# Kernel optimization log

Measured on AMD Instinct MI355X. Metric: run time of the kernel, lower is better.

## Reference

```python
import jax, jax.numpy as jnp
import numpy as np

N_BISECT_ITERS = 50  # entmax library default


def entmax_bisect(X, alpha, n_iter=N_BISECT_ITERS):
    """alpha-entmax over last axis via bisection (Peters & Martins 2019).
    Solves for tau s.t. sum(max((alpha-1)X - tau, 0)^(1/(alpha-1))) = 1."""
    am1 = alpha - 1.0
    inv = 1.0 / am1
    Xa = X * am1
    max_val = jnp.max(Xa, axis=-1, keepdims=True)
    d = X.shape[-1]
    tau_lo = max_val - 1.0                                   # _gp(1, alpha) = 1
    tau_hi = max_val - jnp.asarray(1.0 / d, X.dtype) ** am1  # _gp(1/d, alpha)

    def pfun(tau):
        return jnp.maximum(Xa - tau, 0.0) ** inv

    f_lo = jnp.sum(pfun(tau_lo), axis=-1, keepdims=True) - 1.0

    def body(i, carry):
        tau_lo, dm = carry
        dm = dm * 0.5
        tau_m = tau_lo + dm
        f_m = jnp.sum(pfun(tau_m), axis=-1, keepdims=True) - 1.0
        tau_lo = jnp.where(f_m * f_lo >= 0, tau_m, tau_lo)
        return (tau_lo, dm)

    tau_lo, _ = jax.lax.fori_loop(0, n_iter, body, (tau_lo, tau_hi - tau_lo))
    p = pfun(tau_lo)
    return p / jnp.sum(p, axis=-1, keepdims=True)  # ensure_sum_one


def setup_inputs() -> dict:
    master = jax.random.key(0)
    kq, kk, kv = jax.random.split(master, 3)
    B, H, S, D = 4, 16, 2048, 64
    return {
        "query": jax.random.normal(kq, (B, H, S, D), jnp.float32),
        "key": jax.random.normal(kk, (B, H, S, D), jnp.float32),
        "value": jax.random.normal(kv, (B, H, S, D), jnp.float32),
        "alpha": jnp.float32(1.5),  # canonical entmax-1.5
    }


def reference(query, key, value, alpha):
    D = query.shape[-1]
    scale = 1.0 / jnp.sqrt(jnp.asarray(D, query.dtype))
    scores = jnp.einsum('bhqd,bhkd->bhqk', query, key) * scale  # [B,H,S,S]
    p_attn = entmax_bisect(scores, alpha)
    out = jnp.einsum('bhqk,bhkd->bhqd', p_attn, value)
    return (out, p_attn)
```

## Files before the change

kernel.cpp:

```cpp
#include <hip/hip_runtime.h>
#include <math.h>

#define S_LEN 2048
#define HD    64
#define QT    16
#define NT    1024
#define NW    16
#define NTIL  8
#define CAP   512
#define NITER 28
#define NEWT  10

typedef short s8v __attribute__((ext_vector_type(8)));
typedef float f4v __attribute__((ext_vector_type(4)));

template <bool B> struct BoolT { static constexpr bool value = B; };

__device__ __forceinline__ float wave_sum(float v) {
#pragma unroll
    for (int off = 32; off >= 1; off >>= 1)
        v += __shfl_xor(v, off, 64);
    return v;
}

__device__ __forceinline__ float group16_max(float v) {
#pragma unroll
    for (int off = 8; off >= 1; off >>= 1)
        v = fmaxf(v, __shfl_xor(v, off, 64));
    return v;
}

__device__ __forceinline__ unsigned f2bf2(float lo, float hi) {
    unsigned a = __float_as_uint(lo), b = __float_as_uint(hi);
    a += 0x7FFFu + ((a >> 16) & 1u);
    b += 0x7FFFu + ((b >> 16) & 1u);
    return (a >> 16) | (b & 0xFFFF0000u);
}

__device__ __forceinline__ s8v pack_bf8(const float4& x, const float4& y, float sc) {
    union { s8v s; unsigned u[4]; } f;
    f.u[0] = f2bf2(x.x * sc, x.y * sc);
    f.u[1] = f2bf2(x.z * sc, x.w * sc);
    f.u[2] = f2bf2(y.x * sc, y.y * sc);
    f.u[3] = f2bf2(y.z * sc, y.w * sc);
    return f.s;
}

template <bool INV2>
__device__ __forceinline__ float pfun_t(float t, float inv) {
    float u = fmaxf(t, 0.0f);
    return INV2 ? u * u : powf(u, inv);
}

template <int NR>
__device__ __forceinline__ void newton_reg(const float* cvrow, int ncp, int lane,
                                           float tau0, float& tau_out, float& isum_out) {
    float c[NR];
#pragma unroll
    for (int j = 0; j < NR; ++j) {
        int i = lane + 64 * j;
        c[j] = (i < ncp) ? cvrow[i] : -3.0e38f;
    }
    float tau = tau0;
#pragma unroll
    for (int it = 0; it < NEWT; ++it) {
        float s1 = 0.0f, s2 = 0.0f;
#pragma unroll
        for (int j = 0; j < NR; ++j) {
            float u = fmaxf(c[j] - tau, 0.0f);
            s1 += u;
            s2 = fmaf(u, u, s2);
        }
#pragma unroll
        for (int off = 32; off >= 1; off >>= 1) {
            s1 += __shfl_xor(s1, off, 64);
            s2 += __shfl_xor(s2, off, 64);
        }
        tau += (s2 - 1.0f) * 0.5f * __builtin_amdgcn_rcpf(fmaxf(s1, 1e-30f));
    }
    float s = 0.0f;
#pragma unroll
    for (int j = 0; j < NR; ++j) {
        float u = fmaxf(c[j] - tau, 0.0f);
        s = fmaf(u, u, s);
    }
    s = wave_sum(s);
    tau_out = tau;
    isum_out = 1.0f / s;
}

template <int NR, bool INV2>
__device__ __forceinline__ void bisect_reg(const float* cvrow, int ncp, int lane,
                                           float tau_lo0, float tau_hi, float inv,
                                           float& tau_out, float& isum_out) {
    float c[NR];
#pragma unroll
    for (int j = 0; j < NR; ++j) {
        int i = lane + 64 * j;
        c[j] = (i < ncp) ? cvrow[i] : -3.0e38f;
    }
    float tau = tau_lo0;
    float s0 = 0.0f;
#pragma unroll
    for (int j = 0; j < NR; ++j) s0 += pfun_t<INV2>(c[j] - tau, inv);
    const float f_lo = wave_sum(s0) - 1.0f;
    float dm = tau_hi - tau_lo0;
    for (int it = 0; it < NITER; ++it) {
        dm *= 0.5f;
        float tm = tau + dm;
        float s = 0.0f;
#pragma unroll
        for (int j = 0; j < NR; ++j) s += pfun_t<INV2>(c[j] - tm, inv);
        float fm = wave_sum(s) - 1.0f;
        if (fm * f_lo >= 0.0f) tau = tm;
    }
    float s = 0.0f;
#pragma unroll
    for (int j = 0; j < NR; ++j) s += pfun_t<INV2>(c[j] - tau, inv);
    float ssum = wave_sum(s);
    tau_out = tau;
    isum_out = 1.0f / ssum;
}

__global__ __launch_bounds__(256)
void pack_kv(const float* __restrict__ Kp, const float* __restrict__ Vp,
             s8v* __restrict__ Kb, s8v* __restrict__ Vb, int nK) {
    int idx = blockIdx.x * 256 + threadIdx.x;
    if (idx < nK) {
        const int lane = idx & 63, frag = (idx >> 6) & 1, tile = (idx >> 7) & 127, bh = idx >> 14;
        const int l16 = lane & 15, quad = lane >> 4;
        const float* src = Kp + ((size_t)(bh * S_LEN + tile * 16 + l16)) * HD + frag * 32 + quad * 8;
        float4 a = *(const float4*)src;
        float4 b = *(const float4*)(src + 4);
        Kb[idx] = pack_bf8(a, b, 1.0f);
    } else {
        int v = idx - nK;
        const int lane = v & 63, dt = (v >> 6) & 3, kt32 = (v >> 8) & 63, bh = v >> 14;
        const int l16 = lane & 15, quad = lane >> 4;
        const int base_row = (kt32 >> 2) * 128 + (kt32 & 3) * 4 + quad;
        const float* src = Vp + ((size_t)(bh * S_LEN + base_row)) * HD + dt * 16 + l16;
        float w[8];
#pragma unroll
        for (int j = 0; j < 8; ++j) w[j] = src[(size_t)j * 16 * HD];
        float4 a = {w[0], w[1], w[2], w[3]};
        float4 b = {w[4], w[5], w[6], w[7]};
        Vb[v] = pack_bf8(a, b, 1.0f);
    }
}

template <bool PREK, bool DPV>
__global__ __launch_bounds__(NT)
void entmax_attn(const float* __restrict__ Qp, const float* __restrict__ Kp,
                 const float* __restrict__ Vp, const float* __restrict__ alphap,
                 float* __restrict__ outp, float* __restrict__ pattn,
                 const s8v* __restrict__ Kbf, const s8v* __restrict__ Vbf) {
    constexpr int SM_BIG = DPV ? (NW * QT * 68 * 4)
                               : (QT * CAP * 4 + QT * CAP * 2);
    __shared__ __align__(16) char smem[SM_BIG];
    float          (*candv)[CAP] = (float(*)[CAP])smem;
    unsigned short (*candi)[CAP] = (unsigned short(*)[CAP])(smem + QT * CAP * 4);

    __shared__ int   ncnt[QT];
    __shared__ float rmaxw[QT][NW];
    __shared__ float rmxf[QT];
    __shared__ float taus[QT];
    __shared__ float isums[QT];
    __shared__ float redw[NW];

    const int tid   = threadIdx.x;
    const int wv    = tid >> 6;
    const int lane  = tid & 63;
    const int quad  = lane >> 4;
    const int l16   = lane & 15;
    const int bh    = blockIdx.y;
    const int q0    = blockIdx.x * QT;
    const int wcol0 = wv * (NTIL * 16);

    const float alpha = alphap[0];
    const float am1   = alpha - 1.0f;
    const float inv   = 1.0f / am1;
    const bool  inv2  = (inv == 2.0f);
    const float xscale = (1.0f / sqrtf((float)HD)) * am1;
    const float gp_d   = powf(1.0f / (float)S_LEN, am1);

    if (tid < QT) ncnt[tid] = 0;

    const float* vbase = Vp + (size_t)bh * S_LEN * HD;

    s8v qa0, qa1;
    {
        const float* qp = Qp + ((size_t)bh * S_LEN + q0 + l16) * HD + quad * 8;
        float4 x0 = *(const float4*)qp;
        float4 x1 = *(const float4*)(qp + 4);
        float4 y0 = *(const float4*)(qp + 32);
        float4 y1 = *(const float4*)(qp + 36);
        qa0 = pack_bf8(x0, x1, xscale);
        qa1 = pack_bf8(y0, y1, xscale);
    }

    f4v xa[NTIL];
    if constexpr (PREK) {
        const s8v* kf = Kbf + ((size_t)bh * (S_LEN / 16) + (wcol0 >> 4)) * 2 * 64 + lane;
#pragma unroll
        for (int t = 0; t < NTIL; ++t) {
            s8v kb0 = kf[(2 * t    ) * 64];
            s8v kb1 = kf[(2 * t + 1) * 64];
            f4v acc = {0.0f, 0.0f, 0.0f, 0.0f};
            acc = __builtin_amdgcn_mfma_f32_16x16x32_bf16(qa0, kb0, acc, 0, 0, 0);
            acc = __builtin_amdgcn_mfma_f32_16x16x32_bf16(qa1, kb1, acc, 0, 0, 0);
            xa[t] = acc;
        }
    } else {
        const float* kbase = Kp + (size_t)bh * S_LEN * HD;
#pragma unroll
        for (int t = 0; t < NTIL; ++t) {
            const float* kp = kbase + ((size_t)(wcol0 + t * 16 + l16)) * HD + quad * 8;
            float4 k0 = *(const float4*)kp;
            float4 k1 = *(const float4*)(kp + 4);
            s8v kb0 = pack_bf8(k0, k1, 1.0f);
            f4v acc = {0.0f, 0.0f, 0.0f, 0.0f};
            acc = __builtin_amdgcn_mfma_f32_16x16x32_bf16(qa0, kb0, acc, 0, 0, 0);
            float4 k2 = *(const float4*)(kp + 32);
            float4 k3 = *(const float4*)(kp + 36);
            s8v kb1 = pack_bf8(k2, k3, 1.0f);
            acc = __builtin_amdgcn_mfma_f32_16x16x32_bf16(qa1, kb1, acc, 0, 0, 0);
            xa[t] = acc;
        }
    }

#pragma unroll
    for (int g = 0; g < 4; ++g) {
        float pm = xa[0][g];
#pragma unroll
        for (int t = 1; t < NTIL; ++t) pm = fmaxf(pm, xa[t][g]);
        pm = group16_max(pm);
        if (l16 == 0) rmaxw[quad * 4 + g][wv] = pm;
    }
    __syncthreads();
    if (tid < QT) {
        float m = rmaxw[tid][0];
#pragma unroll
        for (int w = 1; w < NW; ++w) m = fmaxf(m, rmaxw[tid][w]);
        rmxf[tid] = m;
    }
    __syncthreads();

#pragma unroll
    for (int g = 0; g < 4; ++g) {
        const int   row = quad * 4 + g;
        const float thr = rmxf[row] - 1.0f;
        int total = 0;
#pragma unroll
        for (int t = 0; t < NTIL; ++t) {
            unsigned long long m = __ballot(xa[t][g] > thr);
            total += __popc((unsigned)((m >> (quad * 16)) & 0xFFFFull));
        }
        int base = 0;
        if (l16 == 0 && total) base = atomicAdd(&ncnt[row], total);
        base = __shfl(base, quad * 16, 64);
#pragma unroll
        for (int t = 0; t < NTIL; ++t) {
            const float v = xa[t][g];
            const bool pred = (v > thr);
            unsigned long long m = __ballot(pred);
            unsigned gm16 = (unsigned)((m >> (quad * 16)) & 0xFFFFull);
            if (pred) {
                int pos = base + __popc(gm16 & ((1u << l16) - 1u));
                if (pos < CAP) {
                    candv[row][pos] = v;
                    if constexpr (!DPV) candi[row][pos] = (unsigned short)(wcol0 + t * 16 + l16);
                }
            }
            base += __popc(gm16);
        }
    }
    __syncthreads();

    auto tail = [&](auto inv2c) {
        constexpr bool INV2 = decltype(inv2c)::value;

        {
            const int row = wv;
            const int nc = ncnt[row];
            if (nc <= CAP) {
                const int ncp = (nc + 7) & ~7;
                for (int i = nc + lane; i < ncp; i += 64) {
                    candv[row][i] = -3.0e38f;
                    if constexpr (!DPV) candi[row][i] = 0;
                }
                const float mx  = rmxf[row];
                const float tl0 = mx - 1.0f;
                const float th  = mx - gp_d;
                float tau, isum;
                if constexpr (INV2) {
                    if (ncp <= 256) newton_reg<4>(&candv[row][0], ncp, lane, tl0, tau, isum);
                    else            newton_reg<8>(&candv[row][0], ncp, lane, tl0, tau, isum);
                } else {
                    if (ncp <= 256) bisect_reg<4, INV2>(&candv[row][0], ncp, lane, tl0, th, inv, tau, isum);
                    else            bisect_reg<8, INV2>(&candv[row][0], ncp, lane, tl0, th, inv, tau, isum);
                }
                if (lane == 0) { taus[row] = tau; isums[row] = isum; }
            }
        }

#pragma unroll 1
        for (int r = 0; r < QT; ++r) {
            if (ncnt[r] > CAP) {
                const float mx = rmxf[r];
                const int g = r & 3;
                const bool mine = (quad == (r >> 2));
                float tau = mx - 1.0f;
                float s0 = 0.0f;
                if (mine) {
#pragma unroll
                    for (int t = 0; t < NTIL; ++t) s0 += pfun_t<INV2>(xa[t][g] - tau, inv);
                }
                s0 = wave_sum(s0);
                if (lane == 0) redw[wv] = s0;
                __syncthreads();
                float f_lo = -1.0f;
                for (int w = 0; w < NW; ++w) f_lo += redw[w];
                __syncthreads();
                float dm = (mx - gp_d) - tau;
                for (int it = 0; it < NITER; ++it) {
                    dm *= 0.5f;
                    float tm = tau + dm;
                    float s = 0.0f;
                    if (mine) {
#pragma unroll
                        for (int t = 0; t < NTIL; ++t) s += pfun_t<INV2>(xa[t][g] - tm, inv);
                    }
                    s = wave_sum(s);
                    if (lane == 0) redw[wv] = s;
                    __syncthreads();
                    float fm = -1.0f;
                    for (int w = 0; w < NW; ++w) fm += redw[w];
                    __syncthreads();
                    if (fm * f_lo >= 0.0f) tau = tm;
                }
                float s = 0.0f;
                if (mine) {
#pragma unroll
                    for (int t = 0; t < NTIL; ++t) s += pfun_t<INV2>(xa[t][g] - tau, inv);
                }
                s = wave_sum(s);
                if (lane == 0) redw[wv] = s;
                __syncthreads();
                float ssum = 0.0f;
                for (int w = 0; w < NW; ++w) ssum += redw[w];
                __syncthreads();
                if (tid == 0) { taus[r] = tau; isums[r] = 1.0f / ssum; }
            }
        }
        __syncthreads();

        if constexpr (DPV) {
            unsigned short* pwf = (unsigned short*)smem + wv * 2048;
            const size_t prow_base = ((size_t)bh * S_LEN + q0) * S_LEN;
#pragma unroll
            for (int g = 0; g < 4; ++g) {
                const int row = quad * 4 + g;
                const float tau  = taus[row];
                const float isum = isums[row];
                float* prow = pattn + prow_base + (size_t)row * S_LEN + wcol0 + l16;
                union { s8v s; unsigned u[4]; } pk;
                float pprev = 0.0f;
#pragma unroll
                for (int t = 0; t < NTIL; ++t) {
                    float p2 = pfun_t<INV2>(xa[t][g] - tau, inv);
                    prow[t * 16] = p2 * isum;
                    if (t & 1) pk.u[t >> 1] = f2bf2(pprev, p2);
                    else       pprev = p2;
                }
                const int c = (l16 ^ row) & 15;
                *(s8v*)&pwf[row * 128 + c * 8] = pk.s;
            }
            s8v afrag[4];
#pragma unroll
            for (int kt = 0; kt < 4; ++kt) {
                const int c = ((kt * 4 + quad) ^ l16) & 15;
                afrag[kt] = *(const s8v*)&pwf[l16 * 128 + c * 8];
            }
            const s8v* vf = Vbf + ((size_t)bh * (S_LEN / 32) + (wcol0 >> 5)) * 4 * 64 + lane;
            f4v oacc[4];
#pragma unroll
            for (int dt = 0; dt < 4; ++dt) oacc[dt] = (f4v){0.0f, 0.0f, 0.0f, 0.0f};
#pragma unroll
            for (int kt = 0; kt < 4; ++kt) {
#pragma unroll
                for (int dt = 0; dt < 4; ++dt) {
                    s8v b = vf[(kt * 4 + dt) * 64];
                    oacc[dt] = __builtin_amdgcn_mfma_f32_16x16x32_bf16(afrag[kt], b, oacc[dt], 0, 0, 0);
                }
            }
            __syncthreads();
            float* part = (float*)smem;
#pragma unroll
            for (int dt = 0; dt < 4; ++dt) {
#pragma unroll
                for (int g = 0; g < 4; ++g) {
                    part[wv * (QT * 68) + (quad * 4 + g) * 68 + dt * 16 + l16] = oacc[dt][g];
                }
            }
            __syncthreads();
            float s = 0.0f;
#pragma unroll
            for (int w = 0; w < NW; ++w) s += part[w * (QT * 68) + wv * 68 + lane];
            outp[((size_t)bh * S_LEN + q0 + wv) * HD + lane] = s * isums[wv];
        } else {
            const size_t prow_base = ((size_t)bh * S_LEN + q0) * S_LEN;
#pragma unroll
            for (int g = 0; g < 4; ++g) {
                const int row = quad * 4 + g;
                const float tau  = taus[row];
                const float isum = isums[row];
                float* prow = pattn + prow_base + (size_t)row * S_LEN + wcol0 + l16;
#pragma unroll
                for (int t = 0; t < NTIL; ++t) {
                    prow[t * 16] = pfun_t<INV2>(xa[t][g] - tau, inv) * isum;
                }
            }
            __threadfence_block();
            __syncthreads();

            const int row  = wv;
            const int qrow = q0 + row;
            const int nc   = ncnt[row];
            const float tau  = taus[row];
            const float isum = isums[row];
            float oacc = 0.0f;
            if (nc <= CAP) {
                const int ncp = (nc + 7) & ~7;
                for (int i = lane; i < ncp; i += 64)
                    candv[row][i] = pfun_t<INV2>(candv[row][i] - tau, inv);
                float oacc1 = 0.0f;
                for (int i = 0; i < ncp; i += 8) {
#pragma unroll
                    for (int u = 0; u < 8; u += 2) {
                        oacc  = fmaf(candv[row][i + u],
                                     vbase[(size_t)candi[row][i + u] * HD + lane], oacc);
                        oacc1 = fmaf(candv[row][i + u + 1],
                                     vbase[(size_t)candi[row][i + u + 1] * HD + lane], oacc1);
                    }
                }
                oacc = (oacc + oacc1) * isum;
            } else {
                const float* prow = pattn + ((size_t)bh * S_LEN + qrow) * S_LEN;
                for (int k = 0; k < S_LEN; ++k)
                    oacc = fmaf(prow[k], vbase[(size_t)k * HD + lane], oacc);
            }
            outp[((size_t)bh * S_LEN + qrow) * HD + lane] = oacc;
        }
    };

    if (inv2) tail(BoolT<true>{});
    else      tail(BoolT<false>{});
}

extern "C" void kernel_launch(void* const* d_in, const int* in_sizes, int n_in,
                              void* d_out, int out_size, void* d_ws, size_t ws_size,
                              hipStream_t stream) {
    const float* Q = (const float*)d_in[0];
    const float* K = (const float*)d_in[1];
    const float* V = (const float*)d_in[2];
    const float* A = (const float*)d_in[3];
    float* out = (float*)d_out;
    const int BH = in_sizes[0] / (S_LEN * HD);
    float* p = out + (size_t)BH * S_LEN * HD;
    dim3 grid(S_LEN / QT, BH);

    const size_t kb_bytes = (size_t)BH * S_LEN * HD * sizeof(short);
    const int nK = BH * (S_LEN / 16) * 2 * 64;
    const int nV = BH * (S_LEN / 32) * 4 * 64;

    if (d_ws != nullptr && ws_size >= 2 * kb_bytes) {
        s8v* Kb = (s8v*)d_ws;
        s8v* Vb = (s8v*)((char*)d_ws + kb_bytes);
        pack_kv<<<dim3((nK + nV) / 256), 256, 0, stream>>>(K, V, Kb, Vb, nK);
        entmax_attn<true, true><<<grid, NT, 0, stream>>>(Q, K, V, A, out, p, Kb, Vb);
    } else if (d_ws != nullptr && ws_size >= kb_bytes) {
        s8v* Kb = (s8v*)d_ws;
        pack_kv<<<dim3(nK / 256), 256, 0, stream>>>(K, V, Kb, nullptr, nK);
        entmax_attn<true, false><<<grid, NT, 0, stream>>>(Q, K, V, A, out, p, Kb, nullptr);
    } else {
        entmax_attn<false, false><<<grid, NT, 0, stream>>>(Q, K, V, A, out, p, nullptr, nullptr);
    }
}
```

Measured before the change: 1.908 ms.

## Use nontemporal stores, fewer Newton steps, and simplify candidate counting and padding

Switches the attention-probability and output stores in the DPV path to nontemporal stores, so the large p_attn write stream bypasses cache retention. Reduces Newton iterations from 10 to 8 and drops the padding loop for the DPV case by bounding candidate loads by the exact count. Ballot counting now computes all four quad popcounts with 64-bit popcount and then selects one, instead of shifting the mask by a lane-dependent amount. Fewer Newton steps risk a slightly less converged tau.

```diff
diff --git a/kernel.cpp b/kernel.cpp
--- a/kernel.cpp
+++ b/kernel.cpp
@@ -9,7 +9,7 @@
 #define NTIL  8
 #define CAP   512
 #define NITER 28
-#define NEWT  10
+#define NEWT  8
 
 typedef short s8v __attribute__((ext_vector_type(8)));
 typedef float f4v __attribute__((ext_vector_type(4)));
@@ -53,13 +53,13 @@
 }
 
 template <int NR>
-__device__ __forceinline__ void newton_reg(const float* cvrow, int ncp, int lane,
+__device__ __forceinline__ void newton_reg(const float* cvrow, int nc, int lane,
                                            float tau0, float& tau_out, float& isum_out) {
     float c[NR];
 #pragma unroll
     for (int j = 0; j < NR; ++j) {
         int i = lane + 64 * j;
-        c[j] = (i < ncp) ? cvrow[i] : -3.0e38f;
+        c[j] = (i < nc) ? cvrow[i] : -3.0e38f;
     }
     float tau = tau0;
 #pragma unroll
@@ -90,14 +90,14 @@
 }
 
 template <int NR, bool INV2>
-__device__ __forceinline__ void bisect_reg(const float* cvrow, int ncp, int lane,
+__device__ __forceinline__ void bisect_reg(const float* cvrow, int nc, int lane,
                                            float tau_lo0, float tau_hi, float inv,
                                            float& tau_out, float& isum_out) {
     float c[NR];
 #pragma unroll
     for (int j = 0; j < NR; ++j) {
         int i = lane + 64 * j;
-        c[j] = (i < ncp) ? cvrow[i] : -3.0e38f;
+        c[j] = (i < nc) ? cvrow[i] : -3.0e38f;
     }
     float tau = tau_lo0;
     float s0 = 0.0f;
@@ -249,12 +249,17 @@
     for (int g = 0; g < 4; ++g) {
         const int   row = quad * 4 + g;
         const float thr = rmxf[row] - 1.0f;
-        int total = 0;
+        unsigned tq0 = 0, tq1 = 0, tq2 = 0, tq3 = 0;
 #pragma unroll
         for (int t = 0; t < NTIL; ++t) {
             unsigned long long m = __ballot(xa[t][g] > thr);
-            total += __popc((unsigned)((m >> (quad * 16)) & 0xFFFFull));
-        }
+            tq0 += (unsigned)__popcll(m & 0x000000000000FFFFull);
+            tq1 += (unsigned)__popcll(m & 0x00000000FFFF0000ull);
+            tq2 += (unsigned)__popcll(m & 0x0000FFFF00000000ull);
+            tq3 += (unsigned)__popcll(m >> 48);
+        }
+        const int total = (quad & 2) ? ((quad & 1) ? (int)tq3 : (int)tq2)
+                                     : ((quad & 1) ? (int)tq1 : (int)tq0);
         int base = 0;
         if (l16 == 0 && total) base = atomicAdd(&ncnt[row], total);
         base = __shfl(base, quad * 16, 64);
@@ -283,21 +288,23 @@
             const int row = wv;
             const int nc = ncnt[row];
             if (nc <= CAP) {
-                const int ncp = (nc + 7) & ~7;
-                for (int i = nc + lane; i < ncp; i += 64) {
-                    candv[row][i] = -3.0e38f;
-                    if constexpr (!DPV) candi[row][i] = 0;
+                if constexpr (!DPV) {
+                    const int ncp = (nc + 7) & ~7;
+                    for (int i = nc + lane; i < ncp; i += 64) {
+                        candv[row][i] = -3.0e38f;
+                        candi[row][i] = 0;
+                    }
                 }
                 const float mx  = rmxf[row];
                 const float tl0 = mx - 1.0f;
                 const float th  = mx - gp_d;
                 float tau, isum;
                 if constexpr (INV2) {
-                    if (ncp <= 256) newton_reg<4>(&candv[row][0], ncp, lane, tl0, tau, isum);
-                    else            newton_reg<8>(&candv[row][0], ncp, lane, tl0, tau, isum);
+                    if (nc <= 256) newton_reg<4>(&candv[row][0], nc, lane, tl0, tau, isum);
+                    else           newton_reg<8>(&candv[row][0], nc, lane, tl0, tau, isum);
                 } else {
-                    if (ncp <= 256) bisect_reg<4, INV2>(&candv[row][0], ncp, lane, tl0, th, inv, tau, isum);
-                    else            bisect_reg<8, INV2>(&candv[row][0], ncp, lane, tl0, th, inv, tau, isum);
+                    if (nc <= 256) bisect_reg<4, INV2>(&candv[row][0], nc, lane, tl0, th, inv, tau, isum);
+                    else           bisect_reg<8, INV2>(&candv[row][0], nc, lane, tl0, th, inv, tau, isum);
                 }
                 if (lane == 0) { taus[row] = tau; isums[row] = isum; }
             }
@@ -368,7 +375,7 @@
 #pragma unroll
                 for (int t = 0; t < NTIL; ++t) {
                     float p2 = pfun_t<INV2>(xa[t][g] - tau, inv);
-                    prow[t * 16] = p2 * isum;
+                    __builtin_nontemporal_store(p2 * isum, &prow[t * 16]);
                     if (t & 1) pk.u[t >> 1] = f2bf2(pprev, p2);
                     else       pprev = p2;
                 }
@@ -406,7 +413,8 @@
             float s = 0.0f;
 #pragma unroll
             for (int w = 0; w < NW; ++w) s += part[w * (QT * 68) + wv * 68 + lane];
-            outp[((size_t)bh * S_LEN + q0 + wv) * HD + lane] = s * isums[wv];
+            __builtin_nontemporal_store(s * isums[wv],
+                &outp[((size_t)bh * S_LEN + q0 + wv) * HD + lane]);
         } else {
             const size_t prow_base = ((size_t)bh * S_LEN + q0) * S_LEN;
 #pragma unroll
```

Result: faster. 1.870 ms (-2.0%).
